# Kernel optimization log

Hardware: AMD Instinct MI355X
Metric: run time of the kernel (lower is better)

Reference implementation:

```python
import jax, jax.numpy as jnp
import numpy as np

N = 100000      # nodes
E = 1600000     # edges (before self-loops)
F_IN = 16       # num_node_features
HID = 16        # hid
HEADS = 4       # in_head == out_head
B = 64          # num graphs
G = 16          # num_global_features
NEG_SLOPE = 0.2


def gat_conv(x, src, dst, W, a_src, a_dst, b, concat):
    """PyG-style GATConv. x:[N,F], W:[F,H*C], a_src/a_dst:[H,C], b:[H*C] or [C]."""
    n = x.shape[0]
    H, C = a_src.shape
    h = (x @ W).reshape(n, H, C)                       # [N,H,C]
    alpha_s = (h * a_src).sum(-1)                      # [N,H]
    alpha_d = (h * a_dst).sum(-1)                      # [N,H]
    e = jax.nn.leaky_relu(alpha_s[src] + alpha_d[dst], NEG_SLOPE)  # [E',H]
    # segment softmax over destination nodes (stable; max is grad-free)
    m = jax.lax.stop_gradient(jax.ops.segment_max(e, dst, num_segments=n))
    ex = jnp.exp(e - m[dst])
    denom = jax.ops.segment_sum(ex, dst, num_segments=n)
    alpha = ex / (denom[dst] + 1e-16)                  # [E',H]
    out = jax.ops.segment_sum(h[src] * alpha[:, :, None], dst, num_segments=n)  # [N,H,C]
    out = out.reshape(n, H * C) if concat else out.mean(axis=1)
    return out + b


def setup_inputs() -> dict:
    key = jax.random.key(0)
    ks = jax.random.split(key, 24)
    s = 0.1
    inp = {
        "x": jax.random.normal(ks[0], (N, F_IN), jnp.float32),
        "stats": jax.random.normal(ks[1], (B, G), jnp.float32),
        # conv1: F_IN -> HID, heads=HEADS, concat=True
        "W1": jax.random.normal(ks[2], (F_IN, HEADS * HID), jnp.float32) * s,
        "a1s": jax.random.normal(ks[3], (HEADS, HID), jnp.float32) * s,
        "a1d": jax.random.normal(ks[4], (HEADS, HID), jnp.float32) * s,
        "b1": jnp.zeros((HEADS * HID,), jnp.float32),
        # conv2: HID*HEADS -> HID, heads=HEADS, concat=False
        "W2": jax.random.normal(ks[5], (HEADS * HID, HEADS * HID), jnp.float32) * s,
        "a2s": jax.random.normal(ks[6], (HEADS, HID), jnp.float32) * s,
        "a2d": jax.random.normal(ks[7], (HEADS, HID), jnp.float32) * s,
        "b2": jnp.zeros((HID,), jnp.float32),
        # conv3: HID -> HID, heads=HEADS, concat=False
        "W3": jax.random.normal(ks[8], (HID, HEADS * HID), jnp.float32) * s,
        "a3s": jax.random.normal(ks[9], (HEADS, HID), jnp.float32) * s,
        "a3d": jax.random.normal(ks[10], (HEADS, HID), jnp.float32) * s,
        "b3": jnp.zeros((HID,), jnp.float32),
        # MLP head
        "fw1": jax.random.normal(ks[11], (HID + G, 32), jnp.float32) * s,
        "fb1": jnp.zeros((32,), jnp.float32),
        "fw2": jax.random.normal(ks[12], (32, 16), jnp.float32) * s,
        "fb2": jnp.zeros((16,), jnp.float32),
        "fw3": jax.random.normal(ks[13], (16, 1), jnp.float32) * s,
        "fb3": jnp.zeros((1,), jnp.float32),
        "edge_index": jax.random.randint(ks[14], (2, E), 0, N, jnp.int64),
        "batch": jnp.sort(jax.random.randint(ks[15], (N,), 0, B, jnp.int64)),
    }
    return inp


def reference(x, stats, W1, a1s, a1d, b1, W2, a2s, a2d, b2, W3, a3s, a3d, b3,
              fw1, fb1, fw2, fb2, fw3, fb3, edge_index, batch):
    n = x.shape[0]
    loops = jnp.arange(n, dtype=edge_index.dtype)
    src = jnp.concatenate([edge_index[0], loops])  # add_self_loops=True (PyG default)
    dst = jnp.concatenate([edge_index[1], loops])
    h = jax.nn.elu(gat_conv(x, src, dst, W1, a1s, a1d, b1, True))
    h = jax.nn.elu(gat_conv(h, src, dst, W2, a2s, a2d, b2, False))
    h = gat_conv(h, src, dst, W3, a3s, a3d, b3, False)
    nb = stats.shape[0]
    pooled = jax.ops.segment_sum(h, batch, num_segments=nb)
    counts = jax.ops.segment_sum(jnp.ones((n,), h.dtype), batch, num_segments=nb)
    pooled = pooled / jnp.maximum(counts, 1.0)[:, None]   # global_mean_pool
    z = jnp.concatenate([pooled, stats], axis=1)
    z = jax.nn.relu(z @ fw1 + fb1)
    z = jax.nn.relu(z @ fw2 + fb2)
    return z @ fw3 + fb3
```

## Files before the change

### kernel.cpp

```cpp
#include <hip/hip_runtime.h>
#include <hip/hip_bf16.h>
#include <hip/hip_fp16.h>

#define NNODES 100000
#define NEDGES 1600000
#define NHEADS 4
#define NHID   16
#define NB     64
#define NG     16
#define POOL_BLOCKS 256
#define POOL_SLOTS (NB * NG + NB)

#define BKT_SHIFT 7
#define NPB 128
#define NBKT ((NNODES + NPB - 1) / NPB)
#define BCAP 4096
#define SCAT_BLOCKS 256
#define NL1_BLOCKS 2048

typedef float vf2 __attribute__((ext_vector_type(2)));

__device__ __forceinline__ float leaky02(float v) {
    return v > 0.0f ? v : 0.2f * v;
}

__device__ __forceinline__ unsigned char cvt_fp8(float a) {
    int r = __builtin_amdgcn_cvt_pk_fp8_f32(a, a, 0, false);
    return (unsigned char)(r & 0xFF);
}

__device__ __forceinline__ float4 loadQ4(const unsigned char* p) {
    int u = *(const int*)p;
    vf2 lo = __builtin_amdgcn_cvt_pk_f32_fp8(u, false);
    vf2 hi = __builtin_amdgcn_cvt_pk_f32_fp8(u, true);
    return make_float4(lo.x, lo.y, hi.x, hi.y);
}

__device__ __forceinline__ void storeH4(__half* p, float4 v) {
    __half2 a = __floats2half2_rn(v.x, v.y);
    __half2 b = __floats2half2_rn(v.z, v.w);
    uint2 raw;
    raw.x = *reinterpret_cast<unsigned*>(&a);
    raw.y = *reinterpret_cast<unsigned*>(&b);
    *(uint2*)p = raw;
}

template <int FIN>
__device__ __forceinline__ void nl_body_f32(const float* __restrict__ X,
                                            const float* __restrict__ W,
                                            const float* __restrict__ a_s,
                                            const float* __restrict__ a_d,
                                            unsigned char* __restrict__ H,
                                            float* __restrict__ AS,
                                            float* __restrict__ AD, int n,
                                            int wave0, int nwaves, int lane) {
    int head = lane >> 4;
    float w[FIN];
#pragma unroll
    for (int k = 0; k < FIN; ++k) w[k] = W[k * 64 + lane];
    float asl = a_s[lane], adl = a_d[lane];

    for (int i = wave0; i < n; i += nwaves) {
        const float* __restrict__ xr = X + (size_t)i * FIN;
        float acc = 0.0f;
#pragma unroll
        for (int k = 0; k < FIN; ++k) acc += xr[k] * w[k];
        H[(size_t)i * 64 + lane] = cvt_fp8(acc);
        float s1 = acc * asl, s2 = acc * adl;
#pragma unroll
        for (int off = 1; off < 16; off <<= 1) {
            s1 += __shfl_xor(s1, off);
            s2 += __shfl_xor(s2, off);
        }
        if ((lane & 15) == 0) {
            AS[(size_t)i * 4 + head] = s1;
            AD[(size_t)i * 4 + head] = s2;
        }
    }
}

template <int FIN>
__global__ void node_linear3(const float* __restrict__ X,
                             const float* __restrict__ W,
                             const float* __restrict__ a_s,
                             const float* __restrict__ a_d,
                             unsigned char* __restrict__ H,
                             float* __restrict__ AS,
                             float* __restrict__ AD, int n) {
    int lane = threadIdx.x & 63;
    int wave = __builtin_amdgcn_readfirstlane(
        (int)((blockIdx.x * blockDim.x + threadIdx.x) >> 6));
    int nwaves = (gridDim.x * blockDim.x) >> 6;
    nl_body_f32<FIN>(X, W, a_s, a_d, H, AS, AD, n, wave, nwaves, lane);
}

template <int FIN>
__global__ void node_linear3h(const unsigned* __restrict__ X,
                              const float* __restrict__ W,
                              const float* __restrict__ a_s,
                              const float* __restrict__ a_d,
                              unsigned char* __restrict__ H,
                              float* __restrict__ AS,
                              float* __restrict__ AD, int n) {
    int lane = threadIdx.x & 63;
    int head = lane >> 4;
    int wave = __builtin_amdgcn_readfirstlane(
        (int)((blockIdx.x * blockDim.x + threadIdx.x) >> 6));
    int nwaves = (gridDim.x * blockDim.x) >> 6;

    float w[FIN];
#pragma unroll
    for (int k = 0; k < FIN; ++k) w[k] = W[k * 64 + lane];
    float asl = a_s[lane], adl = a_d[lane];

    for (int i = wave; i < n; i += nwaves) {
        const unsigned* __restrict__ xr = X + (size_t)i * (FIN / 2);
        float acc = 0.0f;
#pragma unroll
        for (int k = 0; k < FIN / 2; ++k) {
            unsigned u = xr[k];
            __half2 hh = *reinterpret_cast<const __half2*>(&u);
            float2 f = __half22float2(hh);
            acc += f.x * w[2 * k] + f.y * w[2 * k + 1];
        }
        H[(size_t)i * 64 + lane] = cvt_fp8(acc);
        float s1 = acc * asl, s2 = acc * adl;
#pragma unroll
        for (int off = 1; off < 16; off <<= 1) {
            s1 += __shfl_xor(s1, off);
            s2 += __shfl_xor(s2, off);
        }
        if ((lane & 15) == 0) {
            AS[(size_t)i * 4 + head] = s1;
            AD[(size_t)i * 4 + head] = s2;
        }
    }
}

__global__ void scatter_nl1(const int* __restrict__ src,
                            const int* __restrict__ dst,
                            int* __restrict__ bucketCnt,
                            unsigned int* __restrict__ pairs, int ne,
                            const float* __restrict__ X,
                            const float* __restrict__ W,
                            const float* __restrict__ a_s,
                            const float* __restrict__ a_d,
                            unsigned char* __restrict__ H,
                            float* __restrict__ AS,
                            float* __restrict__ AD, int n) {
    __shared__ int hist[NBKT];
    __shared__ int base[NBKT];
    int tid = threadIdx.x;

    if (blockIdx.x >= SCAT_BLOCKS) {
        int lane = tid & 63;
        int wave = __builtin_amdgcn_readfirstlane(
            (int)(((blockIdx.x - SCAT_BLOCKS) * blockDim.x + tid) >> 6));
        int nwaves = (NL1_BLOCKS * 256) >> 6;
        nl_body_f32<16>(X, W, a_s, a_d, H, AS, AD, n, wave, nwaves, lane);
        return;
    }

    for (int i = tid; i < NBKT; i += 256) hist[i] = 0;
    __syncthreads();

    int chunk = (ne + SCAT_BLOCKS - 1) / SCAT_BLOCKS;
    int beg = blockIdx.x * chunk;
    int end = min(beg + chunk, ne);

    for (int e0 = beg; e0 < end; e0 += 1024) {
        int d[4];
#pragma unroll
        for (int q = 0; q < 4; ++q) {
            int e = e0 + q * 256 + tid;
            d[q] = (e < end) ? dst[e] : -1;
        }
#pragma unroll
        for (int q = 0; q < 4; ++q)
            if (d[q] >= 0) atomicAdd(&hist[d[q] >> BKT_SHIFT], 1);
    }
    __syncthreads();

    for (int i = tid; i < NBKT; i += 256) {
        int h = hist[i];
        base[i] = h ? atomicAdd(&bucketCnt[i], h) : 0;
        hist[i] = 0;
    }
    __syncthreads();

    for (int e0 = beg; e0 < end; e0 += 1024) {
        int d[4], s[4];
#pragma unroll
        for (int q = 0; q < 4; ++q) {
            int e = e0 + q * 256 + tid;
            d[q] = (e < end) ? dst[e] : -1;
            s[q] = (e < end) ? src[e] : 0;
        }
        int r[4], bkt[4];
#pragma unroll
        for (int q = 0; q < 4; ++q) {
            if (d[q] >= 0) {
                bkt[q] = d[q] >> BKT_SHIFT;
                r[q] = base[bkt[q]] + atomicAdd(&hist[bkt[q]], 1);
            }
        }
#pragma unroll
        for (int q = 0; q < 4; ++q) {
            if (d[q] >= 0 && r[q] < BCAP)
                pairs[(size_t)bkt[q] * BCAP + r[q]] =
                    (unsigned)s[q] | ((unsigned)(d[q] & (NPB - 1)) << 20);
        }
    }
}

__global__ void bucket_sort(const unsigned int* __restrict__ pairs,
                            const int* __restrict__ bucketCnt,
                            int* __restrict__ srcs,
                            int* __restrict__ indptr, int n) {
    __shared__ int hist[NPB];
    __shared__ int offl[NPB];
    __shared__ int cur[NPB];
    __shared__ int red[256];
    __shared__ int lsrc[BCAP];
    int bkt = blockIdx.x;
    int t = threadIdx.x;
    int cnt = min(bucketCnt[bkt], BCAP);

    int partial = 0;
    for (int j = t; j < bkt; j += 256) partial += min(bucketCnt[j], BCAP);
    red[t] = partial;
    if (t < NPB) hist[t] = 0;
    __syncthreads();
    for (int s = 128; s > 0; s >>= 1) {
        if (t < s) red[t] += red[t + s];
        __syncthreads();
    }
    int boff = red[0];
    if (bkt == NBKT - 1 && t == 0) indptr[n] = boff + cnt;

    const unsigned int* __restrict__ p = pairs + (size_t)bkt * BCAP;
    unsigned int v[BCAP / 256];
#pragma unroll
    for (int i = 0; i < BCAP / 256; ++i) {
        int e = i * 256 + t;
        v[i] = 0u;
        if (e < cnt) {
            v[i] = p[e];
            atomicAdd(&hist[v[i] >> 20], 1);
        }
    }
    __syncthreads();
    if (t < NPB) offl[t] = hist[t];
    __syncthreads();
    for (int off = 1; off < NPB; off <<= 1) {
        int x = 0;
        if (t < NPB && t >= off) x = offl[t - off];
        __syncthreads();
        if (t < NPB && t >= off) offl[t] += x;
        __syncthreads();
    }
    if (t < NPB) {
        int ex = offl[t] - hist[t];
        cur[t] = ex;
        int node = bkt * NPB + t;
        if (node < n) indptr[node] = boff + ex;
    }
    __syncthreads();
#pragma unroll
    for (int i = 0; i < BCAP / 256; ++i) {
        int e = i * 256 + t;
        if (e < cnt) {
            int r = atomicAdd(&cur[v[i] >> 20], 1);
            lsrc[r] = (int)(v[i] & 0xFFFFFu);
        }
    }
    __syncthreads();
    for (int e = t; e < cnt; e += 256) srcs[boff + e] = lsrc[e];
}

template <int MODE, typename TOUT>
__global__ void gat_pull3(const unsigned char* __restrict__ H,
                          const float* __restrict__ AS,
                          const float* __restrict__ AD,
                          const int* __restrict__ indptr,
                          const int* __restrict__ srcs,
                          const float* __restrict__ bias,
                          TOUT* __restrict__ out, int n) {
    int lane = threadIdx.x & 63;
    int grp  = lane >> 4;
    int sl   = lane & 15;
    int head = sl >> 2;
    int wave = (blockIdx.x * blockDim.x + threadIdx.x) >> 6;
    int nwaves = (gridDim.x * blockDim.x) >> 6;

    for (int d0 = wave * 4; d0 < n; d0 += nwaves * 4) {
        int d = d0 + grp;
        if (d < n) {
            float ad  = AD[(size_t)d * 4 + head];
            float asd = AS[(size_t)d * 4 + head];
            float t0 = asd + ad;
            float wself = __expf(t0 > 0.f ? t0 : 0.2f * t0);
            float den = wself;
            float4 h4s = loadQ4(H + (size_t)d * 64 + sl * 4);
            float4 acc = {wself * h4s.x, wself * h4s.y,
                          wself * h4s.z, wself * h4s.w};

            int beg = indptr[d], end = indptr[d + 1];
            for (int e0 = beg; e0 < end; e0 += 16) {
                int cnt = min(16, end - e0);
                int myS = (sl < cnt) ? srcs[e0 + sl] : 0;
                int j = 0;
                for (; j + 4 <= cnt; j += 4) {
                    int s[4]; float a[4]; float4 h4[4];
#pragma unroll
                    for (int q = 0; q < 4; ++q)
                        s[q] = __shfl(myS, (grp << 4) + j + q);
#pragma unroll
                    for (int q = 0; q < 4; ++q)
                        a[q] = AS[(size_t)s[q] * 4 + head];
#pragma unroll
                    for (int q = 0; q < 4; ++q)
                        h4[q] = loadQ4(H + (size_t)s[q] * 64 + sl * 4);
#pragma unroll
                    for (int q = 0; q < 4; ++q) {
                        float t = a[q] + ad;
                        float w = __expf(t > 0.f ? t : 0.2f * t);
                        den += w;
                        acc.x += w * h4[q].x; acc.y += w * h4[q].y;
                        acc.z += w * h4[q].z; acc.w += w * h4[q].w;
                    }
                }
                for (; j < cnt; ++j) {
                    int s = __shfl(myS, (grp << 4) + j);
                    float t = AS[(size_t)s * 4 + head] + ad;
                    float w = __expf(t > 0.f ? t : 0.2f * t);
                    den += w;
                    float4 h4 = loadQ4(H + (size_t)s * 64 + sl * 4);
                    acc.x += w * h4.x; acc.y += w * h4.y;
                    acc.z += w * h4.z; acc.w += w * h4.w;
                }
            }
            float inv = 1.0f / (den + 1e-16f);
            float4 v = {acc.x * inv, acc.y * inv, acc.z * inv, acc.w * inv};
            if (MODE == 0) {
                float4 b4 = *(const float4*)(bias + sl * 4);
                v.x += b4.x; v.y += b4.y; v.z += b4.z; v.w += b4.w;
                v.x = v.x > 0.f ? v.x : __expf(v.x) - 1.f;
                v.y = v.y > 0.f ? v.y : __expf(v.y) - 1.f;
                v.z = v.z > 0.f ? v.z : __expf(v.z) - 1.f;
                v.w = v.w > 0.f ? v.w : __expf(v.w) - 1.f;
                storeH4((__half*)out + (size_t)d * 64 + sl * 4, v);
            } else {
#pragma unroll
                for (int off = 4; off <= 8; off <<= 1) {
                    v.x += __shfl_xor(v.x, off);
                    v.y += __shfl_xor(v.y, off);
                    v.z += __shfl_xor(v.z, off);
                    v.w += __shfl_xor(v.w, off);
                }
                float4 b4 = *(const float4*)(bias + (sl & 3) * 4);
                v.x = 0.25f * v.x + b4.x; v.y = 0.25f * v.y + b4.y;
                v.z = 0.25f * v.z + b4.z; v.w = 0.25f * v.w + b4.w;
                if (MODE == 1) {
                    v.x = v.x > 0.f ? v.x : __expf(v.x) - 1.f;
                    v.y = v.y > 0.f ? v.y : __expf(v.y) - 1.f;
                    v.z = v.z > 0.f ? v.z : __expf(v.z) - 1.f;
                    v.w = v.w > 0.f ? v.w : __expf(v.w) - 1.f;
                }
                if (sl < 4)
                    *(float4*)((float*)out + (size_t)d * 16 + sl * 4) = v;
            }
        }
    }
}

__global__ void pool_stage1(const float* __restrict__ Hf,
                            const int* __restrict__ batch,
                            float* __restrict__ partials, int n) {
    __shared__ float lp[POOL_SLOTS];
    int tid = threadIdx.x;
    for (int i = tid; i < POOL_SLOTS; i += 256) lp[i] = 0.0f;
    __syncthreads();

    int chunk = (n + POOL_BLOCKS - 1) / POOL_BLOCKS;
    int start = blockIdx.x * chunk;
    int end = min(start + chunk, n);
    int c = tid & 15;
    for (int node = start + (tid >> 4); node < end; node += 16) {
        int b = batch[node];
        atomicAdd(&lp[b * 16 + c], Hf[(size_t)node * 16 + c]);
        if (c == 0) atomicAdd(&lp[NB * NG + b], 1.0f);
    }
    __syncthreads();
    float* outp = partials + (size_t)blockIdx.x * POOL_SLOTS;
    for (int i = tid; i < POOL_SLOTS; i += 256) outp[i] = lp[i];
}

__global__ void pool_stage2(const float* __restrict__ partials,
                            float* __restrict__ pooled_counts) {
    int idx = blockIdx.x * blockDim.x + threadIdx.x;
    if (idx >= POOL_SLOTS) return;
    float s = 0.0f;
    for (int j = 0; j < POOL_BLOCKS; ++j)
        s += partials[(size_t)j * POOL_SLOTS + idx];
    pooled_counts[idx] = s;
}

__global__ void mlp_head(const float* __restrict__ pooled_counts,
                         const float* __restrict__ stats,
                         const float* __restrict__ fw1, const float* __restrict__ fb1,
                         const float* __restrict__ fw2, const float* __restrict__ fb2,
                         const float* __restrict__ fw3, const float* __restrict__ fb3,
                         float* __restrict__ out) {
    int g = threadIdx.x;
    if (g >= NB) return;
    const float* pooled = pooled_counts;
    const float* counts = pooled_counts + NB * NG;
    float z[32];
    float inv = 1.0f / fmaxf(counts[g], 1.0f);
#pragma unroll
    for (int c = 0; c < 16; ++c) z[c] = pooled[g * 16 + c] * inv;
#pragma unroll
    for (int c = 0; c < 16; ++c) z[16 + c] = stats[g * 16 + c];

    float z1[32];
#pragma unroll
    for (int j = 0; j < 32; ++j) {
        float acc = fb1[j];
        for (int k = 0; k < 32; ++k) acc += z[k] * fw1[k * 32 + j];
        z1[j] = fmaxf(acc, 0.0f);
    }
    float z2[16];
#pragma unroll
    for (int j = 0; j < 16; ++j) {
        float acc = fb2[j];
        for (int k = 0; k < 32; ++k) acc += z1[k] * fw2[k * 16 + j];
        z2[j] = fmaxf(acc, 0.0f);
    }
    float acc = fb3[0];
#pragma unroll
    for (int k = 0; k < 16; ++k) acc += z2[k] * fw3[k];
    out[g] = acc;
}

extern "C" void kernel_launch(void* const* d_in, const int* in_sizes, int n_in,
                              void* d_out, int out_size, void* d_ws, size_t ws_size,
                              hipStream_t stream) {
    const float* x    = (const float*)d_in[0];
    const float* stats= (const float*)d_in[1];
    const float* W1   = (const float*)d_in[2];
    const float* a1s  = (const float*)d_in[3];
    const float* a1d  = (const float*)d_in[4];
    const float* b1   = (const float*)d_in[5];
    const float* W2   = (const float*)d_in[6];
    const float* a2s  = (const float*)d_in[7];
    const float* a2d  = (const float*)d_in[8];
    const float* b2   = (const float*)d_in[9];
    const float* W3   = (const float*)d_in[10];
    const float* a3s  = (const float*)d_in[11];
    const float* a3d  = (const float*)d_in[12];
    const float* b3   = (const float*)d_in[13];
    const float* fw1  = (const float*)d_in[14];
    const float* fb1  = (const float*)d_in[15];
    const float* fw2  = (const float*)d_in[16];
    const float* fb2  = (const float*)d_in[17];
    const float* fw3  = (const float*)d_in[18];
    const float* fb3  = (const float*)d_in[19];
    const int* ei     = (const int*)d_in[20];
    const int* batch  = (const int*)d_in[21];

    const int n = NNODES, ne = NEDGES;
    const int* srcI = ei;
    const int* dstI = ei + ne;

    float* ws = (float*)d_ws;
    unsigned char* Hq = (unsigned char*)ws;
    float* B    = (float*)(Hq + (size_t)n * 64);
    __half* B16 = (__half*)B;
    float* C2   = B + (size_t)n * 64;
    float* AS   = C2 + (size_t)n * 16;
    float* AD   = AS + (size_t)n * 4;
    float* PC   = AD + (size_t)n * 4;
    float* PART = PC + POOL_SLOTS;
    int* bucketCnt = (int*)(PART + (size_t)POOL_BLOCKS * POOL_SLOTS);
    int* indptr    = bucketCnt + NBKT;
    int* srcs      = indptr + n + 1;
    unsigned int* pairs = (unsigned int*)B;

    const int TB = 256;
    const int nlBlocks   = 2048;
    const int pullBlocks = (n + 15) / 16;

    hipMemsetAsync(bucketCnt, 0, NBKT * sizeof(int), stream);
    scatter_nl1<<<SCAT_BLOCKS + NL1_BLOCKS, TB, 0, stream>>>(
        srcI, dstI, bucketCnt, pairs, ne,
        x, W1, a1s, a1d, Hq, AS, AD, n);
    bucket_sort<<<NBKT, TB, 0, stream>>>(pairs, bucketCnt, srcs, indptr, n);

    gat_pull3<0, __half><<<pullBlocks, TB, 0, stream>>>(Hq, AS, AD, indptr, srcs, b1, B16, n);

    node_linear3h<64><<<nlBlocks, TB, 0, stream>>>((const unsigned*)B16, W2, a2s, a2d, Hq, AS, AD, n);
    gat_pull3<1, float><<<pullBlocks, TB, 0, stream>>>(Hq, AS, AD, indptr, srcs, b2, C2, n);

    node_linear3<16><<<nlBlocks, TB, 0, stream>>>(C2, W3, a3s, a3d, Hq, AS, AD, n);
    gat_pull3<2, float><<<pullBlocks, TB, 0, stream>>>(Hq, AS, AD, indptr, srcs, b3, B, n);

    pool_stage1<<<POOL_BLOCKS, TB, 0, stream>>>(B, batch, PART, n);
    pool_stage2<<<(POOL_SLOTS + TB - 1) / TB, TB, 0, stream>>>(PART, PC);
    mlp_head<<<1, 64, 0, stream>>>(PC, stats, fw1, fb1, fw2, fb2, fw3, fb3,
                                   (float*)d_out);
}
```

Baseline: 327.5 us.

## Process two destination nodes per 16-lane group in GAT pull kernel

Each 16-lane group now handles two consecutive destination nodes, walking their merged contiguous edge range as one stream and routing each edge's weight to one of two accumulators via a split index. The inner gather is unrolled to 8 edges so more independent loads are in flight. The aim is fewer partially filled 16-edge chunks (average degree is about 16) and better memory-level parallelism on the gathers. In exchange it doubles the accumulator registers and FMA work per edge, and halves the grid size.

```diff
diff --git a/kernel.cpp b/kernel.cpp
--- a/kernel.cpp
+++ b/kernel.cpp
@@ -279,7 +279,7 @@
 }
 
 template <int MODE, typename TOUT>
-__global__ void gat_pull3(const unsigned char* __restrict__ H,
+__global__ void gat_pull4(const unsigned char* __restrict__ H,
                           const float* __restrict__ AS,
                           const float* __restrict__ AD,
                           const int* __restrict__ indptr,
@@ -293,53 +293,89 @@
     int wave = (blockIdx.x * blockDim.x + threadIdx.x) >> 6;
     int nwaves = (gridDim.x * blockDim.x) >> 6;
 
-    for (int d0 = wave * 4; d0 < n; d0 += nwaves * 4) {
-        int d = d0 + grp;
-        if (d < n) {
-            float ad  = AD[(size_t)d * 4 + head];
-            float asd = AS[(size_t)d * 4 + head];
-            float t0 = asd + ad;
-            float wself = __expf(t0 > 0.f ? t0 : 0.2f * t0);
-            float den = wself;
-            float4 h4s = loadQ4(H + (size_t)d * 64 + sl * 4);
-            float4 acc = {wself * h4s.x, wself * h4s.y,
-                          wself * h4s.z, wself * h4s.w};
-
-            int beg = indptr[d], end = indptr[d + 1];
-            for (int e0 = beg; e0 < end; e0 += 16) {
-                int cnt = min(16, end - e0);
-                int myS = (sl < cnt) ? srcs[e0 + sl] : 0;
-                int j = 0;
-                for (; j + 4 <= cnt; j += 4) {
-                    int s[4]; float a[4]; float4 h4[4];
-#pragma unroll
-                    for (int q = 0; q < 4; ++q)
-                        s[q] = __shfl(myS, (grp << 4) + j + q);
-#pragma unroll
-                    for (int q = 0; q < 4; ++q)
-                        a[q] = AS[(size_t)s[q] * 4 + head];
-#pragma unroll
-                    for (int q = 0; q < 4; ++q)
-                        h4[q] = loadQ4(H + (size_t)s[q] * 64 + sl * 4);
-#pragma unroll
-                    for (int q = 0; q < 4; ++q) {
-                        float t = a[q] + ad;
-                        float w = __expf(t > 0.f ? t : 0.2f * t);
-                        den += w;
-                        acc.x += w * h4[q].x; acc.y += w * h4[q].y;
-                        acc.z += w * h4[q].z; acc.w += w * h4[q].w;
-                    }
-                }
-                for (; j < cnt; ++j) {
-                    int s = __shfl(myS, (grp << 4) + j);
-                    float t = AS[(size_t)s * 4 + head] + ad;
+    for (int d0 = wave * 8; d0 < n; d0 += nwaves * 8) {
+        int dA = d0 + (grp << 1);
+        int dB = dA + 1;
+        if (dA >= n) continue;
+        bool hasB = (dB < n);
+
+        float adA = AD[(size_t)dA * 4 + head];
+        float adB = hasB ? AD[(size_t)dB * 4 + head] : 0.0f;
+
+        float tA = AS[(size_t)dA * 4 + head] + adA;
+        float wsA = __expf(tA > 0.f ? tA : 0.2f * tA);
+        float denA = wsA;
+        float4 hA = loadQ4(H + (size_t)dA * 64 + sl * 4);
+        float4 accA = {wsA * hA.x, wsA * hA.y, wsA * hA.z, wsA * hA.w};
+
+        float denB = 0.0f;
+        float4 accB = {0.f, 0.f, 0.f, 0.f};
+        if (hasB) {
+            float tB = AS[(size_t)dB * 4 + head] + adB;
+            float wsB = __expf(tB > 0.f ? tB : 0.2f * tB);
+            denB = wsB;
+            float4 hB = loadQ4(H + (size_t)dB * 64 + sl * 4);
+            accB.x = wsB * hB.x; accB.y = wsB * hB.y;
+            accB.z = wsB * hB.z; accB.w = wsB * hB.w;
+        }
+
+        int begA  = indptr[dA];
+        int split = indptr[dA + 1];
+        int endB  = hasB ? indptr[dB + 1] : split;
+
+        for (int e0 = begA; e0 < endB; e0 += 16) {
+            int cnt = min(16, endB - e0);
+            int myS = (sl < cnt) ? srcs[e0 + sl] : 0;
+            int j = 0;
+            for (; j + 8 <= cnt; j += 8) {
+                int s[8]; float a[8]; float4 h4[8];
+#pragma unroll
+                for (int q = 0; q < 8; ++q)
+                    s[q] = __shfl(myS, (grp << 4) + j + q);
+#pragma unroll
+                for (int q = 0; q < 8; ++q)
+                    a[q] = AS[(size_t)s[q] * 4 + head];
+#pragma unroll
+                for (int q = 0; q < 8; ++q)
+                    h4[q] = loadQ4(H + (size_t)s[q] * 64 + sl * 4);
+#pragma unroll
+                for (int q = 0; q < 8; ++q) {
+                    bool isA = (e0 + j + q) < split;
+                    float ad = isA ? adA : adB;
+                    float t = a[q] + ad;
                     float w = __expf(t > 0.f ? t : 0.2f * t);
-                    den += w;
-                    float4 h4 = loadQ4(H + (size_t)s * 64 + sl * 4);
-                    acc.x += w * h4.x; acc.y += w * h4.y;
-                    acc.z += w * h4.z; acc.w += w * h4.w;
+                    float wA = isA ? w : 0.0f;
+                    float wB = w - wA;
+                    denA += wA; denB += wB;
+                    accA.x += wA * h4[q].x; accA.y += wA * h4[q].y;
+                    accA.z += wA * h4[q].z; accA.w += wA * h4[q].w;
+                    accB.x += wB * h4[q].x; accB.y += wB * h4[q].y;
+                    accB.z += wB * h4[q].z; accB.w += wB * h4[q].w;
                 }
             }
+            for (; j < cnt; ++j) {
+                int s = __shfl(myS, (grp << 4) + j);
+                bool isA = (e0 + j) < split;
+                float ad = isA ? adA : adB;
+                float t = AS[(size_t)s * 4 + head] + ad;
+                float w = __expf(t > 0.f ? t : 0.2f * t);
+                float wA = isA ? w : 0.0f;
+                float wB = w - wA;
+                denA += wA; denB += wB;
+                float4 h4 = loadQ4(H + (size_t)s * 64 + sl * 4);
+                accA.x += wA * h4.x; accA.y += wA * h4.y;
+                accA.z += wA * h4.z; accA.w += wA * h4.w;
+                accB.x += wB * h4.x; accB.y += wB * h4.y;
+                accB.z += wB * h4.z; accB.w += wB * h4.w;
+            }
+        }
+
+#pragma unroll
+        for (int m = 0; m < 2; ++m) {
+            int d = (m == 0) ? dA : dB;
+            if (m == 1 && !hasB) break;
+            float den = (m == 0) ? denA : denB;
+            float4 acc = (m == 0) ? accA : accB;
             float inv = 1.0f / (den + 1e-16f);
             float4 v = {acc.x * inv, acc.y * inv, acc.z * inv, acc.w * inv};
             if (MODE == 0) {
@@ -489,7 +525,7 @@
 
     const int TB = 256;
     const int nlBlocks   = 2048;
-    const int pullBlocks = (n + 15) / 16;
+    const int pullBlocks = (n + 31) / 32;
 
     hipMemsetAsync(bucketCnt, 0, NBKT * sizeof(int), stream);
     scatter_nl1<<<SCAT_BLOCKS + NL1_BLOCKS, TB, 0, stream>>>(
@@ -497,13 +533,13 @@
         x, W1, a1s, a1d, Hq, AS, AD, n);
     bucket_sort<<<NBKT, TB, 0, stream>>>(pairs, bucketCnt, srcs, indptr, n);
 
-    gat_pull3<0, __half><<<pullBlocks, TB, 0, stream>>>(Hq, AS, AD, indptr, srcs, b1, B16, n);
+    gat_pull4<0, __half><<<pullBlocks, TB, 0, stream>>>(Hq, AS, AD, indptr, srcs, b1, B16, n);
 
     node_linear3h<64><<<nlBlocks, TB, 0, stream>>>((const unsigned*)B16, W2, a2s, a2d, Hq, AS, AD, n);
-    gat_pull3<1, float><<<pullBlocks, TB, 0, stream>>>(Hq, AS, AD, indptr, srcs, b2, C2, n);
+    gat_pull4<1, float><<<pullBlocks, TB, 0, stream>>>(Hq, AS, AD, indptr, srcs, b2, C2, n);
 
     node_linear3<16><<<nlBlocks, TB, 0, stream>>>(C2, W3, a3s, a3d, Hq, AS, AD, n);
-    gat_pull3<2, float><<<pullBlocks, TB, 0, stream>>>(Hq, AS, AD, indptr, srcs, b3, B, n);
+    gat_pull4<2, float><<<pullBlocks, TB, 0, stream>>>(Hq, AS, AD, indptr, srcs, b3, B, n);
 
     pool_stage1<<<POOL_BLOCKS, TB, 0, stream>>>(B, batch, PART, n);
     pool_stage2<<<(POOL_SLOTS + TB - 1) / TB, TB, 0, stream>>>(PART, PC);
```

Measured after the change: 351.0 us. 1.07x slower.
